# Kernel tuning notes

Measured on AMD Instinct MI355X. Metric: run time of the kernel, lower is better.

Reference implementation:

```python
import jax, jax.numpy as jnp
import numpy as np

B, T, NODES, D = 16, 24, 8192, 128
TP, TPN = 12, 2              # tem_patchsize, tem_patchnum (T = TP*TPN)
P, NPS = 256, 32             # spatial patches (spa_patchnum//factors), tokens/patch (spa_patchsize*factors)
L = 3
TOD, DOW = 288, 7
IN_D, ND, TD, DD = 64, 32, 16, 16   # input/node/tod/dow dims; D = sum
OUT_LEN = 12
EPS = 1e-6


def _ln(x):
    m = jnp.mean(x, axis=-1, keepdims=True)
    v = jnp.var(x, axis=-1, keepdims=True)
    return (x - m) * jax.lax.rsqrt(v + EPS)


def _attn(x, wqkv, bqkv, wp, bp):
    # x: (M, S, D), single-head scaled dot-product attention (timm Attention, eval mode)
    qkv = x @ wqkv + bqkv                                  # (M, S, 3D)
    q, k, v = jnp.split(qkv, 3, axis=-1)
    a = jax.nn.softmax(jnp.einsum('msd,mtd->mst', q, k) * (D ** -0.5), axis=-1)
    return jnp.einsum('mst,mtd->msd', a, v) @ wp + bp


def _mlp(x, w1, b1, w2, b2):
    return jax.nn.gelu(x @ w1 + b1, approximate=False) @ w2 + b2


def setup_inputs() -> dict:
    key = jax.random.key(0)
    ks = iter(jax.random.split(key, 40))
    s = 0.02
    inp = {}
    inp['x'] = jax.random.normal(next(ks), (B, T, NODES, 1), jnp.float32)
    tod_ix = jax.random.randint(next(ks), (B, T, NODES, 1), 0, TOD)
    dow_ix = jax.random.randint(next(ks), (B, T, NODES, 1), 0, DOW)
    inp['te'] = jnp.concatenate([tod_ix, dow_ix], -1).astype(jnp.int64)
    perm = jax.random.permutation(next(ks), NODES)
    inp['reo_all_idx'] = perm.astype(jnp.int64)            # gather order (patched reorder)
    inp['ori_parts_idx'] = jnp.arange(NODES, dtype=jnp.int64)
    inp['reo_parts_idx'] = jnp.argsort(perm).astype(jnp.int64)  # inverse permutation for scatter-back
    inp['w_st'] = jax.random.normal(next(ks), (IN_D, 3, TP)) * s
    inp['b_st'] = jnp.zeros((IN_D,))
    inp['node_emb'] = jax.random.normal(next(ks), (NODES, ND)) * s
    inp['tod_emb'] = jax.random.normal(next(ks), (TOD, TD)) * s
    inp['dow_emb'] = jax.random.normal(next(ks), (DOW, DD)) * s
    for pre in ('s', 'n'):
        inp[pre + '_qkv_w'] = jax.random.normal(next(ks), (L, D, 3 * D)) * s
        inp[pre + '_qkv_b'] = jnp.zeros((L, 3 * D))
        inp[pre + '_proj_w'] = jax.random.normal(next(ks), (L, D, D)) * s
        inp[pre + '_proj_b'] = jnp.zeros((L, D))
        inp[pre + '_fc1_w'] = jax.random.normal(next(ks), (L, D, D)) * s
        inp[pre + '_fc1_b'] = jnp.zeros((L, D))
        inp[pre + '_fc2_w'] = jax.random.normal(next(ks), (L, D, D)) * s
        inp[pre + '_fc2_b'] = jnp.zeros((L, D))
    inp['w_reg'] = jax.random.normal(next(ks), (OUT_LEN, TPN * D)) * s
    inp['b_reg'] = jnp.zeros((OUT_LEN,))
    return inp


def reference(x, te, reo_all_idx, ori_parts_idx, reo_parts_idx,
              w_st, b_st, node_emb, tod_emb, dow_emb,
              s_qkv_w, s_qkv_b, s_proj_w, s_proj_b, s_fc1_w, s_fc1_b, s_fc2_w, s_fc2_b,
              n_qkv_w, n_qkv_b, n_proj_w, n_proj_b, n_fc1_w, n_fc1_b, n_fc2_w, n_fc2_b,
              w_reg, b_reg):
    # ---- embedding ----
    tef = te.astype(jnp.float32)
    x1 = jnp.concatenate([x, tef[..., 0:1] / TOD, tef[..., 1:2] / DOW], -1)   # (B,T,N,3)
    # Conv2d(3->IN_D, kernel (1,TP), stride (1,TP)) == temporal patchify + contraction
    x1 = x1.reshape(B, TPN, TP, NODES, 3)
    h = jnp.einsum('btpnc,dcp->btnd', x1, w_st) + b_st                        # (B,TPN,N,IN_D)
    tid = te[:, -TPN:, :, 0]
    diw = te[:, -TPN:, :, 1]
    nemb = jnp.broadcast_to(node_emb[None, None], (B, TPN, NODES, ND))
    h = jnp.concatenate([h, tod_emb[tid], dow_emb[diw], nemb], -1)            # (B,TPN,N,D)
    # ---- reorder gather into (patches, tokens) ----
    rex = h[:, :, reo_all_idx, :].reshape(B, TPN, P, NPS, D)
    # ---- dual window attention blocks ----
    for i in range(L):
        q = _ln(rex).reshape(B * TPN * P, NPS, D)                             # depth attn within patch
        rex = rex + _attn(q, s_qkv_w[i], s_qkv_b[i], s_proj_w[i], s_proj_b[i]).reshape(B, TPN, P, NPS, D)
        rex = rex + _mlp(_ln(rex), s_fc1_w[i], s_fc1_b[i], s_fc2_w[i], s_fc2_b[i])
        xt = rex.transpose(0, 1, 3, 2, 4)                                     # (B,TPN,NPS,P,D)
        q = _ln(xt).reshape(B * TPN * NPS, P, D)                              # breadth attn across patches
        rex = rex + _attn(q, n_qkv_w[i], n_qkv_b[i], n_proj_w[i], n_proj_b[i]).reshape(B, TPN, NPS, P, D).transpose(0, 1, 3, 2, 4)
        rex = rex + _mlp(_ln(rex), n_fc1_w[i], n_fc1_b[i], n_fc2_w[i], n_fc2_b[i])
    rex = rex.reshape(B, TPN, P * NPS, D)
    # ---- scatter back to original node order ----
    orig = jnp.zeros((B, TPN, NODES, D), rex.dtype).at[:, :, ori_parts_idx, :].set(rex[:, :, reo_parts_idx, :])
    feat = orig.transpose(0, 1, 3, 2).reshape(B, TPN * D, NODES)
    y = jnp.einsum('bcn,oc->bon', feat, w_reg) + b_reg[None, :, None]
    return y[..., None]                                                       # (B, OUT_LEN, NODES, 1)
```

## Files before the change

kernel.cpp:

```cpp
#include <hip/hip_runtime.h>

#define DEV __device__ __forceinline__
typedef __attribute__((ext_vector_type(8))) short s16x8;
typedef __attribute__((ext_vector_type(4))) float f32x4;
typedef __attribute__((ext_vector_type(4))) int i32x4;
typedef unsigned short u16;

#define NB 16
#define TPN 2
#define NODES 8192
#define D 128
#define P 256
#define NPS 32
#define OUT_LEN 12

DEV f32x4 mfma16(s16x8 a, s16x8 b, f32x4 c) {
  return __builtin_amdgcn_mfma_f32_16x16x32_bf16(a, b, c, 0, 0, 0);
}

DEV short f2bf(float f) {
  union { float f; unsigned u; } v; v.f = f;
  unsigned r = v.u + 0x7fffu + ((v.u >> 16) & 1u);
  return (short)(r >> 16);
}
DEV float bf2f(u16 h) {
  union { unsigned u; float f; } v; v.u = ((unsigned)h) << 16; return v.f;
}

DEV int swz256(int row, int b) { return (row << 8) + (b ^ ((row & 7) << 4)); }
DEV int swz512(int row, int b) { return (row << 9) + (b ^ ((row & 7) << 4)); }

DEV s16x8 ldsA(const char* base, int mbase, int kbase, int lane) {
  int row = mbase + (lane & 15);
  int b = (kbase + ((lane >> 4) << 3)) << 1;
  return *(const s16x8*)(base + swz256(row, b));
}

DEV float rowred(float v) {
  v += __shfl_xor(v, 1);
  v += __shfl_xor(v, 2);
  v += __shfl_xor(v, 4);
  v += __shfl_xor(v, 8);
  return v;
}
DEV float gred(float v) {
  v += __shfl_xor(v, 16);
  v += __shfl_xor(v, 32);
  return v;
}

DEV void stageW(char* buf, const u16* __restrict__ w, int tid) {
  int col = tid >> 4, kc = tid & 15;
  s16x8 v = *(const s16x8*)(w + col * 128 + kc * 8);
  *(s16x8*)(buf + swz256(col, kc * 16)) = v;
}

__global__ void k_prep(const float* __restrict__ src, u16* __restrict__ dst, int K, int N) {
  int idx = blockIdx.x * 256 + threadIdx.x;
  int total = 3 * K * N;
  if (idx >= total) return;
  int l = idx / (K * N);
  int r = idx - l * K * N;
  int n = r / K;
  int k = r - n * K;
  dst[idx] = (u16)f2bf(src[l * K * N + k * N + n]);
}

__global__ __launch_bounds__(256) void k_embed(
    const float* __restrict__ x, const int* __restrict__ te, const int* __restrict__ reo_parts,
    const float* __restrict__ w_st, const float* __restrict__ b_st,
    const float* __restrict__ node_emb, const float* __restrict__ tod_emb,
    const float* __restrict__ dow_emb, float* __restrict__ rex) {
  __shared__ float sx[12][16], s0[12][16], s1[12][16];
  __shared__ int sed[2][16];
  __shared__ int sj[16];
  __shared__ float hb[16][132];
  int gid = blockIdx.x;
  int chunk = gid & 511, bt = gid >> 9;
  int b = bt >> 1, tt = bt & 1;
  int tid = threadIdx.x;
  int nl = tid & 15, c = tid >> 4;
  int n = chunk * 16 + nl;
  if (c < 12) {
    size_t off = ((size_t)(b * 24 + tt * 12 + c)) * NODES + n;
    sx[c][nl] = x[off];
    int2 t2 = *(const int2*)(te + 2 * off);
    s0[c][nl] = (float)t2.x * (1.0f / 288.0f);
    s1[c][nl] = (float)t2.y * (1.0f / 7.0f);
  } else if (c == 12) {
    size_t off = ((size_t)(b * 24 + 22 + tt)) * NODES + n;
    int2 t2 = *(const int2*)(te + 2 * off);
    sed[0][nl] = t2.x;
    sed[1][nl] = t2.y;
  } else if (c == 13) {
    sj[nl] = reo_parts[n];
  }
  __syncthreads();
  int db = c * 8;
  float o[8];
#pragma unroll
  for (int dd = 0; dd < 8; ++dd) {
    int d = db + dd;
    float v;
    if (d < 64) {
      float acc = b_st[d];
      const float* wd = w_st + d * 36;
#pragma unroll
      for (int p = 0; p < 12; ++p)
        acc += sx[p][nl] * wd[p] + s0[p][nl] * wd[12 + p] + s1[p][nl] * wd[24 + p];
      v = acc;
    } else if (d < 80) {
      v = tod_emb[sed[0][nl] * 16 + (d - 64)];
    } else if (d < 96) {
      v = dow_emb[sed[1][nl] * 16 + (d - 80)];
    } else {
      v = node_emb[n * 32 + (d - 96)];
    }
    o[dd] = v;
  }
  *(float4*)&hb[nl][db] = make_float4(o[0], o[1], o[2], o[3]);
  *(float4*)&hb[nl][db + 4] = make_float4(o[4], o[5], o[6], o[7]);
  __syncthreads();
  int row = tid >> 4, cw = tid & 15;
  float4 v0 = *(float4*)&hb[row][cw * 8];
  float4 v1 = *(float4*)&hb[row][cw * 8 + 4];
  float* dst = rex + ((size_t)bt * NODES + sj[row]) * D + cw * 8;
  *(float4*)dst = v0;
  *(float4*)(dst + 4) = v1;
}

template <bool CROSS>
__global__ __launch_bounds__(1024, 4) void k_fused(
    float* __restrict__ rex,
    const u16* __restrict__ wqkv, const float* __restrict__ bqkv,
    const u16* __restrict__ wprj, const float* __restrict__ bprj,
    const u16* __restrict__ w1t, const float* __restrict__ b1,
    const u16* __restrict__ w2t, const float* __restrict__ b2) {
  __shared__ __align__(16) char sm[163840];
  char* Kb = sm;
  char* VT = sm + 65536;
  char* WSa = sm + 131072;
  char* WSb = sm + 147456;
  int tid = threadIdx.x;
  int w = tid >> 6, lane = tid & 63;
  int r = lane & 15, g = lane >> 4;
  char* scrQ = sm + 65536 + w * 4096;
  char* Pscr = sm + 131072 + w * 1280;

  int sq = blockIdx.x;
  const int TS = CROSS ? (NPS * D) : D;
  const size_t TSB = (size_t)TS * 4;
  float* Xblk;
  if (CROSS) {
    int bt = sq >> 5, i = sq & 31;
    Xblk = rex + (size_t)bt * (NODES * D) + i * D;
  } else {
    Xblk = rex + (size_t)sq * (256 * D);
  }
  int myrow = w * 16 + r;
  float* XrowG = (float*)((char*)Xblk + (size_t)myrow * TSB);

#pragma unroll
  for (int it = 0; it < 8; ++it) {
    int unit = it * 1024 + tid;
    int row = unit >> 5, col = unit & 31;
    i32x4 v = *(const i32x4*)((const char*)Xblk + (size_t)row * TSB + col * 16);
    *(i32x4*)(sm + (row << 9) + ((col * 16) ^ ((row & 7) << 4))) = v;
  }
  stageW(WSa, wqkv, tid);
  __syncthreads();

  s16x8 ax[4];
  {
    float s = 0.f, s2 = 0.f;
#pragma unroll
    for (int kt = 0; kt < 4; ++kt) {
      f32x4 u0 = *(const f32x4*)(sm + (myrow << 9) + ((kt * 128 + g * 32) ^ ((myrow & 7) << 4)));
      f32x4 u1 = *(const f32x4*)(sm + (myrow << 9) + ((kt * 128 + g * 32 + 16) ^ ((myrow & 7) << 4)));
#pragma unroll
      for (int j = 0; j < 4; ++j) { s += u0[j] + u1[j]; s2 += u0[j] * u0[j] + u1[j] * u1[j]; }
    }
    s = gred(s); s2 = gred(s2);
    float m = s * 0.0078125f;
    float rsd = rsqrtf(s2 * 0.0078125f - m * m + 1e-6f);
#pragma unroll
    for (int kt = 0; kt < 4; ++kt) {
      f32x4 u0 = *(const f32x4*)(sm + (myrow << 9) + ((kt * 128 + g * 32) ^ ((myrow & 7) << 4)));
      f32x4 u1 = *(const f32x4*)(sm + (myrow << 9) + ((kt * 128 + g * 32 + 16) ^ ((myrow & 7) << 4)));
      s16x8 o;
#pragma unroll
      for (int j = 0; j < 4; ++j) {
        o[j] = f2bf((u0[j] - m) * rsd);
        o[j + 4] = f2bf((u1[j] - m) * rsd);
      }
      ax[kt] = o;
    }
  }
  __syncthreads();

  s16x8 aq[4];
  for (int t = 0; t < 6; ++t) {
    const char* cur = (t & 1) ? WSb : WSa;
    if (t < 5) stageW((t & 1) ? WSa : WSb, wqkv + (size_t)(t + 1) * 8192, tid);
#pragma unroll
    for (int sub = 0; sub < 4; ++sub) {
      int colg = t * 64 + sub * 16 + r;
      f32x4 acc = {0.f, 0.f, 0.f, 0.f};
#pragma unroll
      for (int kt = 0; kt < 4; ++kt)
        acc = mfma16(ax[kt], ldsA(cur, sub * 16, kt * 32, lane), acc);
      float bias = bqkv[colg];
#pragma unroll
      for (int e = 0; e < 4; ++e) {
        float v = acc[e] + bias;
        int tok = w * 16 + g * 4 + e;
        if (t < 2) {
          *(u16*)(scrQ + swz256(g * 4 + e, colg * 2)) = (u16)f2bf(v);
        } else if (t < 4) {
          *(u16*)(Kb + swz256(tok, (colg - 128) * 2)) = (u16)f2bf(v);
        } else {
          *(u16*)(VT + swz512(colg - 256, tok * 2)) = (u16)f2bf(v);
        }
      }
    }
    if (t == 1) {
#pragma unroll
      for (int kt = 0; kt < 4; ++kt) aq[kt] = ldsA(scrQ, 0, kt * 32, lane);
    }
    __syncthreads();
  }

  const float scale = 0.08838834764831845f;
  float sum[4] = {0.f, 0.f, 0.f, 0.f};
  f32x4 av[8];
#pragma unroll
  for (int nt = 0; nt < 8; ++nt) av[nt] = (f32x4){0.f, 0.f, 0.f, 0.f};

  if (CROSS) {
    for (int cc = 0; cc < 8; ++cc) {
#pragma unroll
      for (int sub = 0; sub < 2; ++sub) {
        int kt2 = cc * 2 + sub;
        f32x4 acc = {0.f, 0.f, 0.f, 0.f};
#pragma unroll
        for (int kt = 0; kt < 4; ++kt) {
          s16x8 b = ldsA(Kb, kt2 * 16, kt * 32, lane);
          acc = mfma16(aq[kt], b, acc);
        }
#pragma unroll
        for (int e = 0; e < 4; ++e) {
          float p = __expf(acc[e] * scale);
          sum[e] += p;
          *(u16*)(Pscr + (g * 4 + e) * 80 + (sub * 16 + r) * 2) = (u16)f2bf(p);
        }
      }
      s16x8 ap = *(const s16x8*)(Pscr + r * 80 + g * 16);
#pragma unroll
      for (int nt = 0; nt < 8; ++nt) {
        s16x8 bv = *(const s16x8*)(VT + swz512(nt * 16 + r, (cc * 32 + g * 8) * 2));
        av[nt] = mfma16(ap, bv, av[nt]);
      }
    }
  } else {
    int pw = w >> 1;
#pragma unroll
    for (int sub = 0; sub < 2; ++sub) {
      f32x4 acc = {0.f, 0.f, 0.f, 0.f};
#pragma unroll
      for (int kt = 0; kt < 4; ++kt) {
        s16x8 b = ldsA(Kb, pw * 32 + sub * 16, kt * 32, lane);
        acc = mfma16(aq[kt], b, acc);
      }
#pragma unroll
      for (int e = 0; e < 4; ++e) {
        float p = __expf(acc[e] * scale);
        sum[e] += p;
        *(u16*)(Pscr + (g * 4 + e) * 80 + (sub * 16 + r) * 2) = (u16)f2bf(p);
      }
    }
    s16x8 ap = *(const s16x8*)(Pscr + r * 80 + g * 16);
#pragma unroll
    for (int nt = 0; nt < 8; ++nt) {
      s16x8 bv = *(const s16x8*)(VT + swz512(nt * 16 + r, (pw * 32 + g * 8) * 2));
      f32x4 z = {0.f, 0.f, 0.f, 0.f};
      av[nt] = mfma16(ap, bv, z);
    }
  }
#pragma unroll
  for (int e = 0; e < 4; ++e) sum[e] = rowred(sum[e]);
  __syncthreads();

  {
    float rinv[4];
#pragma unroll
    for (int e = 0; e < 4; ++e) rinv[e] = 1.0f / sum[e];
#pragma unroll
    for (int nt = 0; nt < 8; ++nt)
#pragma unroll
      for (int e = 0; e < 4; ++e)
        *(u16*)(Kb + swz256(w * 16 + g * 4 + e, (nt * 16 + r) * 2)) =
            (u16)f2bf(av[nt][e] * rinv[e]);
  }

  stageW(WSa, wprj, tid);
  __syncthreads();
#pragma unroll
  for (int t = 0; t < 2; ++t) {
    const char* cur = t ? WSb : WSa;
    if (t == 0) stageW(WSb, wprj + 8192, tid);
#pragma unroll
    for (int sub = 0; sub < 4; ++sub) {
      int colg = t * 64 + sub * 16 + r;
      f32x4 acc = {0.f, 0.f, 0.f, 0.f};
#pragma unroll
      for (int kt = 0; kt < 4; ++kt)
        acc = mfma16(ldsA(Kb, w * 16, kt * 32, lane), ldsA(cur, sub * 16, kt * 32, lane), acc);
      float bias = bprj[colg];
#pragma unroll
      for (int e = 0; e < 4; ++e)
        *(u16*)(VT + swz256(w * 16 + g * 4 + e, colg * 2)) = (u16)f2bf(acc[e] + bias);
    }
    __syncthreads();
  }

  {
    float s = 0.f, s2 = 0.f;
#pragma unroll
    for (int kt = 0; kt < 4; ++kt) {
      float4 a = *(const float4*)(XrowG + kt * 32 + g * 8);
      float4 b = *(const float4*)(XrowG + kt * 32 + g * 8 + 4);
      s16x8 d = *(const s16x8*)(VT + swz256(myrow, (kt * 32 + g * 8) * 2));
      float v0 = a.x + bf2f((u16)d[0]), v1 = a.y + bf2f((u16)d[1]);
      float v2 = a.z + bf2f((u16)d[2]), v3 = a.w + bf2f((u16)d[3]);
      float v4 = b.x + bf2f((u16)d[4]), v5 = b.y + bf2f((u16)d[5]);
      float v6 = b.z + bf2f((u16)d[6]), v7 = b.w + bf2f((u16)d[7]);
      *(float4*)(XrowG + kt * 32 + g * 8) = make_float4(v0, v1, v2, v3);
      *(float4*)(XrowG + kt * 32 + g * 8 + 4) = make_float4(v4, v5, v6, v7);
      s += v0 + v1 + v2 + v3 + v4 + v5 + v6 + v7;
      s2 += v0 * v0 + v1 * v1 + v2 * v2 + v3 * v3 + v4 * v4 + v5 * v5 + v6 * v6 + v7 * v7;
    }
    s = gred(s); s2 = gred(s2);
    float m = s * 0.0078125f;
    float rsd = rsqrtf(s2 * 0.0078125f - m * m + 1e-6f);
#pragma unroll
    for (int kt = 0; kt < 4; ++kt) {
      float4 a = *(const float4*)(XrowG + kt * 32 + g * 8);
      float4 b = *(const float4*)(XrowG + kt * 32 + g * 8 + 4);
      s16x8 o;
      o[0] = f2bf((a.x - m) * rsd); o[1] = f2bf((a.y - m) * rsd);
      o[2] = f2bf((a.z - m) * rsd); o[3] = f2bf((a.w - m) * rsd);
      o[4] = f2bf((b.x - m) * rsd); o[5] = f2bf((b.y - m) * rsd);
      o[6] = f2bf((b.z - m) * rsd); o[7] = f2bf((b.w - m) * rsd);
      *(s16x8*)(Kb + swz256(myrow, (kt * 32 + g * 8) * 2)) = o;
    }
  }

  stageW(WSa, w1t, tid);
  __syncthreads();
#pragma unroll
  for (int t = 0; t < 2; ++t) {
    const char* cur = t ? WSb : WSa;
    if (t == 0) stageW(WSb, w1t + 8192, tid);
#pragma unroll
    for (int sub = 0; sub < 4; ++sub) {
      int colg = t * 64 + sub * 16 + r;
      f32x4 acc = {0.f, 0.f, 0.f, 0.f};
#pragma unroll
      for (int kt = 0; kt < 4; ++kt)
        acc = mfma16(ldsA(Kb, w * 16, kt * 32, lane), ldsA(cur, sub * 16, kt * 32, lane), acc);
      float bias = b1[colg];
#pragma unroll
      for (int e = 0; e < 4; ++e) {
        float v0 = acc[e] + bias;
        v0 = 0.5f * v0 * (1.0f + erff(v0 * 0.70710678118654752f));
        *(u16*)(VT + swz256(w * 16 + g * 4 + e, colg * 2)) = (u16)f2bf(v0);
      }
    }
    __syncthreads();
  }

  stageW(WSa, w2t, tid);
  __syncthreads();
#pragma unroll
  for (int t = 0; t < 2; ++t) {
    const char* cur = t ? WSb : WSa;
    if (t == 0) stageW(WSb, w2t + 8192, tid);
#pragma unroll
    for (int sub = 0; sub < 4; ++sub) {
      int colg = t * 64 + sub * 16 + r;
      f32x4 acc = {0.f, 0.f, 0.f, 0.f};
#pragma unroll
      for (int kt = 0; kt < 4; ++kt)
        acc = mfma16(ldsA(VT, w * 16, kt * 32, lane), ldsA(cur, sub * 16, kt * 32, lane), acc);
      float bias = b2[colg];
#pragma unroll
      for (int e = 0; e < 4; ++e)
        *(u16*)(Kb + swz256(w * 16 + g * 4 + e, colg * 2)) = (u16)f2bf(acc[e] + bias);
    }
    if (t == 0) __syncthreads();
  }

#pragma unroll
  for (int kt = 0; kt < 4; ++kt) {
    float4 a = *(const float4*)(XrowG + kt * 32 + g * 8);
    float4 b = *(const float4*)(XrowG + kt * 32 + g * 8 + 4);
    s16x8 d = *(const s16x8*)(Kb + swz256(myrow, (kt * 32 + g * 8) * 2));
    *(float4*)(XrowG + kt * 32 + g * 8) = make_float4(
        a.x + bf2f((u16)d[0]), a.y + bf2f((u16)d[1]),
        a.z + bf2f((u16)d[2]), a.w + bf2f((u16)d[3]));
    *(float4*)(XrowG + kt * 32 + g * 8 + 4) = make_float4(
        b.x + bf2f((u16)d[4]), b.y + bf2f((u16)d[5]),
        b.z + bf2f((u16)d[6]), b.w + bf2f((u16)d[7]));
  }
}

__global__ __launch_bounds__(256) void k_readout(
    const float* __restrict__ rex, const int* __restrict__ ori_idx,
    const int* __restrict__ reo_idx, const float* __restrict__ w_reg,
    const float* __restrict__ b_reg, float* __restrict__ out) {
  __shared__ float wl[3072];
  for (int i2 = threadIdx.x; i2 < 3072; i2 += 256) wl[i2] = w_reg[i2];
  __syncthreads();
  int b = blockIdx.x >> 7;
  int chunk = blockIdx.x & 127;
  int m = chunk * 64 + (threadIdx.x >> 2);
  int q = threadIdx.x & 3;
  int nOut = ori_idx[m];
  int j = reo_idx[m];
  int t = q >> 1;
  const float* src = rex + ((size_t)(b * 2 + t) * NODES + j) * D + (q & 1) * 64;
  float acc[12] = {0.f, 0.f, 0.f, 0.f, 0.f, 0.f, 0.f, 0.f, 0.f, 0.f, 0.f, 0.f};
#pragma unroll
  for (int k = 0; k < 64; k += 4) {
    float4 v = *(const float4*)(src + k);
#pragma unroll
    for (int o = 0; o < 12; ++o) {
      float4 wv = *(const float4*)(&wl[o * 256 + q * 64 + k]);
      acc[o] += v.x * wv.x + v.y * wv.y + v.z * wv.z + v.w * wv.w;
    }
  }
#pragma unroll
  for (int o = 0; o < 12; ++o) {
    acc[o] += __shfl_xor(acc[o], 1);
    acc[o] += __shfl_xor(acc[o], 2);
  }
  if (q == 0) {
#pragma unroll
    for (int o = 0; o < 12; ++o)
      out[((size_t)b * 12 + o) * NODES + nOut] = acc[o] + b_reg[o];
  }
}

extern "C" void kernel_launch(void* const* d_in, const int* in_sizes, int n_in,
                              void* d_out, int out_size, void* d_ws, size_t ws_size,
                              hipStream_t stream) {
  (void)in_sizes; (void)n_in; (void)out_size;
  const float* x = (const float*)d_in[0];
  const int* te = (const int*)d_in[1];
  const int* reo_all = (const int*)d_in[2];
  const int* ori_parts = (const int*)d_in[3];
  const int* reo_parts = (const int*)d_in[4];
  const float* w_st = (const float*)d_in[5];
  const float* b_st = (const float*)d_in[6];
  const float* node_emb = (const float*)d_in[7];
  const float* tod_emb = (const float*)d_in[8];
  const float* dow_emb = (const float*)d_in[9];
  const float* s_qkv_w = (const float*)d_in[10];
  const float* s_qkv_b = (const float*)d_in[11];
  const float* s_proj_w = (const float*)d_in[12];
  const float* s_proj_b = (const float*)d_in[13];
  const float* s_fc1_w = (const float*)d_in[14];
  const float* s_fc1_b = (const float*)d_in[15];
  const float* s_fc2_w = (const float*)d_in[16];
  const float* s_fc2_b = (const float*)d_in[17];
  const float* n_qkv_w = (const float*)d_in[18];
  const float* n_qkv_b = (const float*)d_in[19];
  const float* n_proj_w = (const float*)d_in[20];
  const float* n_proj_b = (const float*)d_in[21];
  const float* n_fc1_w = (const float*)d_in[22];
  const float* n_fc1_b = (const float*)d_in[23];
  const float* n_fc2_w = (const float*)d_in[24];
  const float* n_fc2_b = (const float*)d_in[25];
  const float* w_reg = (const float*)d_in[26];
  const float* b_reg = (const float*)d_in[27];
  (void)reo_all;

  const size_t REX_BYTES = (size_t)NB * TPN * NODES * D * 4;
  if (ws_size < REX_BYTES + 1179648) return;
  float* rex = (float*)d_ws;
  u16* wt = (u16*)((char*)d_ws + REX_BYTES);
  u16* s_qkv_t = wt + 0;
  u16* s_prj_t = wt + 147456;
  u16* s_fc1_t = wt + 196608;
  u16* s_fc2_t = wt + 245760;
  u16* n_qkv_t = wt + 294912;
  u16* n_prj_t = wt + 442368;
  u16* n_fc1_t = wt + 491520;
  u16* n_fc2_t = wt + 540672;

  k_prep<<<(3 * 128 * 384 + 255) / 256, 256, 0, stream>>>(s_qkv_w, s_qkv_t, 128, 384);
  k_prep<<<(3 * 128 * 128 + 255) / 256, 256, 0, stream>>>(s_proj_w, s_prj_t, 128, 128);
  k_prep<<<(3 * 128 * 128 + 255) / 256, 256, 0, stream>>>(s_fc1_w, s_fc1_t, 128, 128);
  k_prep<<<(3 * 128 * 128 + 255) / 256, 256, 0, stream>>>(s_fc2_w, s_fc2_t, 128, 128);
  k_prep<<<(3 * 128 * 384 + 255) / 256, 256, 0, stream>>>(n_qkv_w, n_qkv_t, 128, 384);
  k_prep<<<(3 * 128 * 128 + 255) / 256, 256, 0, stream>>>(n_proj_w, n_prj_t, 128, 128);
  k_prep<<<(3 * 128 * 128 + 255) / 256, 256, 0, stream>>>(n_fc1_w, n_fc1_t, 128, 128);
  k_prep<<<(3 * 128 * 128 + 255) / 256, 256, 0, stream>>>(n_fc2_w, n_fc2_t, 128, 128);

  k_embed<<<NB * TPN * (NODES / 16), 256, 0, stream>>>(
      x, te, reo_parts, w_st, b_st, node_emb, tod_emb, dow_emb, rex);

  for (int l = 0; l < 3; ++l) {
    k_fused<false><<<NB * TPN * (NODES / 256), 1024, 0, stream>>>(
        rex, s_qkv_t + (size_t)l * 49152, s_qkv_b + l * 384,
        s_prj_t + (size_t)l * 16384, s_proj_b + l * 128,
        s_fc1_t + (size_t)l * 16384, s_fc1_b + l * 128,
        s_fc2_t + (size_t)l * 16384, s_fc2_b + l * 128);
    k_fused<true><<<NB * TPN * NPS, 1024, 0, stream>>>(
        rex, n_qkv_t + (size_t)l * 49152, n_qkv_b + l * 384,
        n_prj_t + (size_t)l * 16384, n_proj_b + l * 128,
        n_fc1_t + (size_t)l * 16384, n_fc1_b + l * 128,
        n_fc2_t + (size_t)l * 16384, n_fc2_b + l * 128);
  }

  k_readout<<<NB * (NODES / 64), 256, 0, stream>>>(
      rex, ori_parts, reo_parts, w_reg, b_reg, (float*)d_out);
}
```

Before: 1.875 ms.

## Defer attention residual write and stage both weight halves per GEMM

The block kernel no longer writes the attention residual back to the global row buffer. The projection output stays in LDS as bf16 and is added together with the MLP output in one final residual update. Each projection, fc1 and fc2 GEMM now stages both 64-column weight halves up front and computes all tiles before one barrier, which cuts the number of __syncthreads. The float-to-bf16 conversion is switched to the HIP intrinsic. The trade-off is more LDS staging and register pressure per GEMM, and the two sublayer deltas are summed in bf16 before being added to the residual, which changes rounding.

New measurement: 1.788 ms, median of 3. 1.05x faster.

```diff
diff --git a/kernel.cpp b/kernel.cpp
--- a/kernel.cpp
+++ b/kernel.cpp
@@ -1,4 +1,5 @@
 #include <hip/hip_runtime.h>
+#include <hip/hip_bf16.h>
 
 #define DEV __device__ __forceinline__
 typedef __attribute__((ext_vector_type(8))) short s16x8;
@@ -18,10 +19,11 @@
   return __builtin_amdgcn_mfma_f32_16x16x32_bf16(a, b, c, 0, 0, 0);
 }
 
-DEV short f2bf(float f) {
-  union { float f; unsigned u; } v; v.f = f;
-  unsigned r = v.u + 0x7fffu + ((v.u >> 16) & 1u);
-  return (short)(r >> 16);
+DEV u16 f2bf(float f) {
+  __hip_bfloat16 h = __float2bfloat16(f);
+  u16 u;
+  __builtin_memcpy(&u, &h, 2);
+  return u;
 }
 DEV float bf2f(u16 h) {
   union { unsigned u; float f; } v; v.u = ((unsigned)h) << 16; return v.f;
@@ -63,7 +65,7 @@
   int r = idx - l * K * N;
   int n = r / K;
   int k = r - n * K;
-  dst[idx] = (u16)f2bf(src[l * K * N + k * N + n]);
+  dst[idx] = f2bf(src[l * K * N + k * N + n]);
 }
 
 __global__ __launch_bounds__(256) void k_embed(
@@ -190,8 +192,8 @@
       s16x8 o;
 #pragma unroll
       for (int j = 0; j < 4; ++j) {
-        o[j] = f2bf((u0[j] - m) * rsd);
-        o[j + 4] = f2bf((u1[j] - m) * rsd);
+        o[j] = (short)f2bf((u0[j] - m) * rsd);
+        o[j + 4] = (short)f2bf((u1[j] - m) * rsd);
       }
       ax[kt] = o;
     }
@@ -215,11 +217,11 @@
         float v = acc[e] + bias;
         int tok = w * 16 + g * 4 + e;
         if (t < 2) {
-          *(u16*)(scrQ + swz256(g * 4 + e, colg * 2)) = (u16)f2bf(v);
+          *(u16*)(scrQ + swz256(g * 4 + e, colg * 2)) = f2bf(v);
         } else if (t < 4) {
-          *(u16*)(Kb + swz256(tok, (colg - 128) * 2)) = (u16)f2bf(v);
+          *(u16*)(Kb + swz256(tok, (colg - 128) * 2)) = f2bf(v);
         } else {
-          *(u16*)(VT + swz512(colg - 256, tok * 2)) = (u16)f2bf(v);
+          *(u16*)(VT + swz512(colg - 256, tok * 2)) = f2bf(v);
         }
       }
     }
@@ -251,7 +253,7 @@
         for (int e = 0; e < 4; ++e) {
           float p = __expf(acc[e] * scale);
           sum[e] += p;
-          *(u16*)(Pscr + (g * 4 + e) * 80 + (sub * 16 + r) * 2) = (u16)f2bf(p);
+          *(u16*)(Pscr + (g * 4 + e) * 80 + (sub * 16 + r) * 2) = f2bf(p);
         }
       }
       s16x8 ap = *(const s16x8*)(Pscr + r * 80 + g * 16);
@@ -275,7 +277,7 @@
       for (int e = 0; e < 4; ++e) {
         float p = __expf(acc[e] * scale);
         sum[e] += p;
-        *(u16*)(Pscr + (g * 4 + e) * 80 + (sub * 16 + r) * 2) = (u16)f2bf(p);
+        *(u16*)(Pscr + (g * 4 + e) * 80 + (sub * 16 + r) * 2) = f2bf(p);
       }
     }
     s16x8 ap = *(const s16x8*)(Pscr + r * 80 + g * 16);
@@ -299,29 +301,37 @@
 #pragma unroll
       for (int e = 0; e < 4; ++e)
         *(u16*)(Kb + swz256(w * 16 + g * 4 + e, (nt * 16 + r) * 2)) =
-            (u16)f2bf(av[nt][e] * rinv[e]);
-  }
-
+            f2bf(av[nt][e] * rinv[e]);
+  }
   stageW(WSa, wprj, tid);
-  __syncthreads();
-#pragma unroll
-  for (int t = 0; t < 2; ++t) {
-    const char* cur = t ? WSb : WSa;
-    if (t == 0) stageW(WSb, wprj + 8192, tid);
-#pragma unroll
-    for (int sub = 0; sub < 4; ++sub) {
-      int colg = t * 64 + sub * 16 + r;
-      f32x4 acc = {0.f, 0.f, 0.f, 0.f};
-#pragma unroll
-      for (int kt = 0; kt < 4; ++kt)
-        acc = mfma16(ldsA(Kb, w * 16, kt * 32, lane), ldsA(cur, sub * 16, kt * 32, lane), acc);
-      float bias = bprj[colg];
-#pragma unroll
-      for (int e = 0; e < 4; ++e)
-        *(u16*)(VT + swz256(w * 16 + g * 4 + e, colg * 2)) = (u16)f2bf(acc[e] + bias);
-    }
-    __syncthreads();
-  }
+  stageW(WSb, wprj + 8192, tid);
+  __syncthreads();
+
+  {
+    f32x4 accp[2][4];
+#pragma unroll
+    for (int t = 0; t < 2; ++t)
+#pragma unroll
+      for (int sub = 0; sub < 4; ++sub) {
+        f32x4 acc = {0.f, 0.f, 0.f, 0.f};
+#pragma unroll
+        for (int kt = 0; kt < 4; ++kt)
+          acc = mfma16(ldsA(Kb, w * 16, kt * 32, lane),
+                       ldsA(t ? WSb : WSa, sub * 16, kt * 32, lane), acc);
+        accp[t][sub] = acc;
+      }
+#pragma unroll
+    for (int t = 0; t < 2; ++t)
+#pragma unroll
+      for (int sub = 0; sub < 4; ++sub) {
+        int colg = t * 64 + sub * 16 + r;
+        float bias = bprj[colg];
+#pragma unroll
+        for (int e = 0; e < 4; ++e)
+          *(u16*)(VT + swz256(w * 16 + g * 4 + e, colg * 2)) = f2bf(accp[t][sub][e] + bias);
+      }
+  }
+  __syncthreads();
 
   {
     float s = 0.f, s2 = 0.f;
@@ -334,8 +344,6 @@
       float v2 = a.z + bf2f((u16)d[2]), v3 = a.w + bf2f((u16)d[3]);
       float v4 = b.x + bf2f((u16)d[4]), v5 = b.y + bf2f((u16)d[5]);
       float v6 = b.z + bf2f((u16)d[6]), v7 = b.w + bf2f((u16)d[7]);
-      *(float4*)(XrowG + kt * 32 + g * 8) = make_float4(v0, v1, v2, v3);
-      *(float4*)(XrowG + kt * 32 + g * 8 + 4) = make_float4(v4, v5, v6, v7);
       s += v0 + v1 + v2 + v3 + v4 + v5 + v6 + v7;
       s2 += v0 * v0 + v1 * v1 + v2 * v2 + v3 * v3 + v4 * v4 + v5 * v5 + v6 * v6 + v7 * v7;
     }
@@ -346,65 +354,89 @@
     for (int kt = 0; kt < 4; ++kt) {
       float4 a = *(const float4*)(XrowG + kt * 32 + g * 8);
       float4 b = *(const float4*)(XrowG + kt * 32 + g * 8 + 4);
+      s16x8 d = *(const s16x8*)(VT + swz256(myrow, (kt * 32 + g * 8) * 2));
       s16x8 o;
-      o[0] = f2bf((a.x - m) * rsd); o[1] = f2bf((a.y - m) * rsd);
-      o[2] = f2bf((a.z - m) * rsd); o[3] = f2bf((a.w - m) * rsd);
-      o[4] = f2bf((b.x - m) * rsd); o[5] = f2bf((b.y - m) * rsd);
-      o[6] = f2bf((b.z - m) * rsd); o[7] = f2bf((b.w - m) * rsd);
+      o[0] = (short)f2bf((a.x + bf2f((u16)d[0]) - m) * rsd);
+      o[1] = (short)f2bf((a.y + bf2f((u16)d[1]) - m) * rsd);
+      o[2] = (short)f2bf((a.z + bf2f((u16)d[2]) - m) * rsd);
+      o[3] = (short)f2bf((a.w + bf2f((u16)d[3]) - m) * rsd);
+      o[4] = (short)f2bf((b.x + bf2f((u16)d[4]) - m) * rsd);
+      o[5] = (short)f2bf((b.y + bf2f((u16)d[5]) - m) * rsd);
+      o[6] = (short)f2bf((b.z + bf2f((u16)d[6]) - m) * rsd);
+      o[7] = (short)f2bf((b.w + bf2f((u16)d[7]) - m) * rsd);
       *(s16x8*)(Kb + swz256(myrow, (kt * 32 + g * 8) * 2)) = o;
     }
   }
-
   stageW(WSa, w1t, tid);
-  __syncthreads();
-#pragma unroll
-  for (int t = 0; t < 2; ++t) {
-    const char* cur = t ? WSb : WSa;
-    if (t == 0) stageW(WSb, w1t + 8192, tid);
-#pragma unroll
-    for (int sub = 0; sub < 4; ++sub) {
-      int colg = t * 64 + sub * 16 + r;
-      f32x4 acc = {0.f, 0.f, 0.f, 0.f};
-#pragma unroll
-      for (int kt = 0; kt < 4; ++kt)
-        acc = mfma16(ldsA(Kb, w * 16, kt * 32, lane), ldsA(cur, sub * 16, kt * 32, lane), acc);
-      float bias = b1[colg];
-#pragma unroll
-      for (int e = 0; e < 4; ++e) {
-        float v0 = acc[e] + bias;
-        v0 = 0.5f * v0 * (1.0f + erff(v0 * 0.70710678118654752f));
-        *(u16*)(VT + swz256(w * 16 + g * 4 + e, colg * 2)) = (u16)f2bf(v0);
-      }
-    }
-    __syncthreads();
-  }
-
+  stageW(WSb, w1t + 8192, tid);
+  __syncthreads();
+
+  {
+    f32x4 acc1[2][4];
+#pragma unroll
+    for (int t = 0; t < 2; ++t)
+#pragma unroll
+      for (int sub = 0; sub < 4; ++sub) {
+        f32x4 acc = {0.f, 0.f, 0.f, 0.f};
+#pragma unroll
+        for (int kt = 0; kt < 4; ++kt)
+          acc = mfma16(ldsA(Kb, w * 16, kt * 32, lane),
+                       ldsA(t ? WSb : WSa, sub * 16, kt * 32, lane), acc);
+        acc1[t][sub] = acc;
+      }
+#pragma unroll
+    for (int t = 0; t < 2; ++t)
+#pragma unroll
+      for (int sub = 0; sub < 4; ++sub) {
+        int colg = t * 64 + sub * 16 + r;
+        float bias = b1[colg];
+#pragma unroll
+        for (int e = 0; e < 4; ++e) {
+          float v0 = acc1[t][sub][e] + bias;
+          v0 = 0.5f * v0 * (1.0f + erff(v0 * 0.70710678118654752f));
+          *(u16*)(Kb + swz256(w * 16 + g * 4 + e, colg * 2)) = f2bf(v0);
+        }
+      }
+  }
+  __syncthreads();
   stageW(WSa, w2t, tid);
-  __syncthreads();
-#pragma unroll
-  for (int t = 0; t < 2; ++t) {
-    const char* cur = t ? WSb : WSa;
-    if (t == 0) stageW(WSb, w2t + 8192, tid);
-#pragma unroll
-    for (int sub = 0; sub < 4; ++sub) {
-      int colg = t * 64 + sub * 16 + r;
-      f32x4 acc = {0.f, 0.f, 0.f, 0.f};
-#pragma unroll
-      for (int kt = 0; kt < 4; ++kt)
-        acc = mfma16(ldsA(VT, w * 16, kt * 32, lane), ldsA(cur, sub * 16, kt * 32, lane), acc);
-      float bias = b2[colg];
-#pragma unroll
-      for (int e = 0; e < 4; ++e)
-        *(u16*)(Kb + swz256(w * 16 + g * 4 + e, colg * 2)) = (u16)f2bf(acc[e] + bias);
-    }
-    if (t == 0) __syncthreads();
+  stageW(WSb, w2t + 8192, tid);
+  __syncthreads();
+
+  {
+    f32x4 acc2[2][4];
+#pragma unroll
+    for (int t = 0; t < 2; ++t)
+#pragma unroll
+      for (int sub = 0; sub < 4; ++sub) {
+        f32x4 acc = {0.f, 0.f, 0.f, 0.f};
+#pragma unroll
+        for (int kt = 0; kt < 4; ++kt)
+          acc = mfma16(ldsA(Kb, w * 16, kt * 32, lane),
+                       ldsA(t ? WSb : WSa, sub * 16, kt * 32, lane), acc);
+        acc2[t][sub] = acc;
+      }
+#pragma unroll
+    for (int t = 0; t < 2; ++t)
+#pragma unroll
+      for (int sub = 0; sub < 4; ++sub) {
+        int colg = t * 64 + sub * 16 + r;
+        float bias = b2[colg];
+#pragma unroll
+        for (int e = 0; e < 4; ++e) {
+          int row = w * 16 + g * 4 + e;
+          u16 d1 = *(u16*)(VT + swz256(row, colg * 2));
+          *(u16*)(VT + swz256(row, colg * 2)) =
+              f2bf(acc2[t][sub][e] + bias + bf2f(d1));
+        }
+      }
   }
 
 #pragma unroll
   for (int kt = 0; kt < 4; ++kt) {
     float4 a = *(const float4*)(XrowG + kt * 32 + g * 8);
     float4 b = *(const float4*)(XrowG + kt * 32 + g * 8 + 4);
-    s16x8 d = *(const s16x8*)(Kb + swz256(myrow, (kt * 32 + g * 8) * 2));
+    s16x8 d = *(const s16x8*)(VT + swz256(myrow, (kt * 32 + g * 8) * 2));
     *(float4*)(XrowG + kt * 32 + g * 8) = make_float4(
         a.x + bf2f((u16)d[0]), a.y + bf2f((u16)d[1]),
         a.z + bf2f((u16)d[2]), a.w + bf2f((u16)d[3]));
```
